# Kernel tuning notes

Hardware: AMD Instinct MI355X
Metric: run time of the kernel (lower is better)

Reference implementation:

```python
import jax, jax.numpy as jnp
import numpy as np

B, SQ, SKV = 4, 2048, 2048
DQ, DKV, H, NH = 1024, 1024, 1024, 16
HD = H // NH


def setup_inputs() -> dict:
    key = jax.random.key(0)
    ks = jax.random.split(key, 10)
    s = 0.02
    return {
        "query": jax.random.normal(ks[0], (B, SQ, DQ), jnp.float32),
        "key_value": jax.random.normal(ks[1], (B, SKV, DKV), jnp.float32),
        "Wq": jax.random.normal(ks[2], (DQ, H), jnp.float32) * s,
        "bq": jnp.zeros((H,), jnp.float32),
        "Wk": jax.random.normal(ks[3], (DKV, H), jnp.float32) * s,
        "bk": jnp.zeros((H,), jnp.float32),
        "Wv": jax.random.normal(ks[4], (DKV, H), jnp.float32) * s,
        "bv": jnp.zeros((H,), jnp.float32),
        "Wo": jax.random.normal(ks[5], (H, DQ), jnp.float32) * s,
        "bo": jnp.zeros((DQ,), jnp.float32),
    }


def reference(query, key_value, Wq, bq, Wk, bk, Wv, bv, Wo, bo):
    b, sq, _ = query.shape
    skv = key_value.shape[1]
    scale = np.sqrt(HD).astype(np.float32)
    # project and split heads: [B, S, H] -> [B, NH, S, HD]
    q = (query @ Wq + bq).reshape(b, sq, NH, HD).transpose(0, 2, 1, 3)
    k = (key_value @ Wk + bk).reshape(b, skv, NH, HD).transpose(0, 2, 1, 3)
    v = (key_value @ Wv + bv).reshape(b, skv, NH, HD).transpose(0, 2, 1, 3)
    scores = jnp.einsum("bhqd,bhkd->bhqk", q, k) / scale
    attn = jax.nn.softmax(scores, axis=-1)
    out = jnp.einsum("bhqk,bhkd->bhqd", attn, v)
    out = out.transpose(0, 2, 1, 3).reshape(b, sq, NH * HD)
    return out @ Wo + bo
```

## Files before the change

kernel.cpp:

```cpp
#include <hip/hip_runtime.h>


typedef short s16x8 __attribute__((ext_vector_type(8)));
typedef short s16x4 __attribute__((ext_vector_type(4)));
typedef float f32x4 __attribute__((ext_vector_type(4)));
typedef float f32x16 __attribute__((ext_vector_type(16)));
typedef unsigned short u16;
typedef unsigned int u32;

__device__ __forceinline__ u16 f2bf(float f){
    union{float f;u32 u;} v; v.f=f;
    u32 r = v.u + 0x7fffu + ((v.u>>16)&1u);
    return (u16)(r>>16);
}
__device__ __forceinline__ int swz(int row,int colB){ return row*128 + (colB ^ ((row&7)<<4)); }

__device__ __forceinline__ void gl16(const void* g, void* l){
    __builtin_amdgcn_global_load_lds((__attribute__((address_space(1))) void*)(void*)g,
                                     (__attribute__((address_space(3))) void*)l, 16, 0, 0);
}
__device__ __forceinline__ u32 cvtpk(float lo, float hi){
    u32 r; asm("v_cvt_pk_bf16_f32 %0, %1, %2" : "=v"(r) : "v"(lo), "v"(hi)); return r;
}
__device__ __forceinline__ void plswap(u32& a, u32& b){
    asm("v_permlane32_swap_b32 %0, %1" : "+v"(a), "+v"(b));
}

#define QSCALE 0.1803368801111204f

__global__ __launch_bounds__(256) void cvtbf2(const float* __restrict__ a, const float* __restrict__ b,
                                              u16* __restrict__ oa, u16* __restrict__ ob){
    int blk = blockIdx.x;
    const float* in = a; u16* out = oa;
    if (blk >= 4096){ in = b; out = ob; blk -= 4096; }
    size_t i = ((size_t)blk*256 + threadIdx.x)*8;
    f32x4 x = *(const f32x4*)(in+i), y = *(const f32x4*)(in+i+4);
    s16x8 o;
    #pragma unroll
    for (int j=0;j<4;++j){ o[j]=(short)f2bf(x[j]); o[4+j]=(short)f2bf(y[j]); }
    *(s16x8*)(out+i) = o;
}

__device__ __forceinline__ void transW_body(const float* __restrict__ W, u16* __restrict__ Wt){
    __shared__ u16 T[64*68];
    const int tid = threadIdx.x;
    const int n0 = blockIdx.x*64, k0 = blockIdx.y*64;
    const int tr = tid>>4, tc = (tid&15)*4;
    #pragma unroll
    for (int p=0;p<4;++p){
        int k = p*16 + tr;
        f32x4 v = *(const f32x4*)(W + (size_t)(k0+k)*1024 + n0 + tc);
        s16x4 o;
        #pragma unroll
        for (int j=0;j<4;++j) o[j]=(short)f2bf(v[j]);
        *(s16x4*)(T + k*68 + tc) = o;
    }
    __syncthreads();
    #pragma unroll
    for (int p=0;p<4;++p){
        int n = p*16 + tr;
        s16x4 o;
        #pragma unroll
        for (int e=0;e<4;++e) o[e] = (short)T[(tc+e)*68 + n];
        *(s16x4*)(Wt + (size_t)(n0+n)*1024 + k0 + tc) = o;
    }
}
__global__ __launch_bounds__(256) void transW(const float* __restrict__ W, u16* __restrict__ Wt){
    transW_body(W, Wt);
}
__global__ __launch_bounds__(256) void transW3(const float* __restrict__ W0, const float* __restrict__ W1,
                                               const float* __restrict__ W2,
                                               u16* __restrict__ O0, u16* __restrict__ O1, u16* __restrict__ O2){
    const float* W = blockIdx.z==0 ? W0 : (blockIdx.z==1 ? W1 : W2);
    u16*       Wt = blockIdx.z==0 ? O0 : (blockIdx.z==1 ? O1 : O2);
    transW_body(W, Wt);
}

template<int EPI>
__global__ __launch_bounds__(256)
void gemm128(const u16* __restrict__ A, const u16* __restrict__ Bt,
             const float* __restrict__ bias, void* __restrict__ C,
             int M, int N, int K, float scale)
{
    __shared__ __align__(16) u16 As[2][128*64];
    __shared__ __align__(16) u16 Bs[2][128*64];
    const int tid = threadIdx.x, lane = tid&63, wave = tid>>6;
    const int ln = lane&15, g = lane>>4;
    const int wm = wave>>1, wn = wave&1;
    const int bm = blockIdx.x, bn = blockIdx.y;

    f32x4 acc[4][4] = {};

    const int r0g = tid>>3, cc8 = (tid&7)*8;
    const u16* aA = A  + (size_t)(bm*128 + r0g)*K + cc8;
    const u16* aB = Bt + (size_t)(bn*128 + r0g)*K + cc8;

    auto stage = [&](int k0, int buf){
        char* pa = (char*)As[buf] + tid*16;
        char* pb = (char*)Bs[buf] + tid*16;
        #pragma unroll
        for (int i=0;i<4;++i){
            gl16(aA + k0 + i*32*K, pa + i*4096);
            gl16(aB + k0 + i*32*K, pb + i*4096);
        }
    };

    stage(0, 0);
    int cur = 0;
    for (int k0=0; k0<K; k0+=64){
        if (k0+64 < K){
            stage(k0+64, cur^1);
            asm volatile("s_waitcnt vmcnt(8)" ::: "memory");
        } else {
            asm volatile("s_waitcnt vmcnt(0)" ::: "memory");
        }
        __builtin_amdgcn_s_barrier();
        #pragma unroll
        for (int kk=0;kk<2;++kk){
            s16x8 af[4], bf[4];
            #pragma unroll
            for (int mi=0;mi<4;++mi)
                af[mi] = *(const s16x8*)((const char*)As[cur] + (size_t)(wm*64+mi*16+ln)*128 + kk*64 + g*16);
            #pragma unroll
            for (int ni=0;ni<4;++ni)
                bf[ni] = *(const s16x8*)((const char*)Bs[cur] + (size_t)(wn*64+ni*16+ln)*128 + kk*64 + g*16);
            #pragma unroll
            for (int mi=0;mi<4;++mi)
                #pragma unroll
                for (int ni=0;ni<4;++ni)
                    acc[mi][ni] = __builtin_amdgcn_mfma_f32_16x16x32_bf16(af[mi], bf[ni], acc[mi][ni], 0,0,0);
        }
        __builtin_amdgcn_s_barrier();
        cur ^= 1;
    }

    #pragma unroll
    for (int mi=0;mi<4;++mi){
        #pragma unroll
        for (int ni=0;ni<4;++ni){
            int col = bn*128 + wn*64 + ni*16 + ln;
            float bv = bias[col];
            #pragma unroll
            for (int r=0;r<4;++r){
                int row = bm*128 + wm*64 + mi*16 + 4*g + r;
                float v = (acc[mi][ni][r] + bv) * scale;
                if constexpr (EPI==0)
                    ((u16*)C)[(size_t)row*N + col] = f2bf(v);
                else if constexpr (EPI==2){
                    int b = row>>11, s = row&2047;
                    ((u16*)C)[((size_t)(b*1024 + col))*2048 + s] = f2bf(v);
                } else
                    ((float*)C)[(size_t)row*N + col] = v;
            }
        }
    }
}

template<bool A_IS_F32, int EPI>
__global__ __launch_bounds__(256)
void gemm_bias_64(const void* __restrict__ Av, const float* __restrict__ W,
                  const float* __restrict__ bias, void* __restrict__ Cout,
                  int M, int N, int K, float scale)
{
    __shared__ __align__(16) char smem[16384];
    char* As = smem;
    char* Ws = smem + 8192;
    const int tid  = threadIdx.x;
    const int lane = tid & 63, wave = tid >> 6;
    const int g = lane >> 4, ln = lane & 15;
    const int wm = wave >> 1, wn = wave & 1;
    const int bm = blockIdx.x, bn = blockIdx.y;
    f32x4 acc[2][2] = {};
    const int srow = tid >> 2;
    const int sch  = (tid & 3) * 16;

    for (int k0 = 0; k0 < K; k0 += 64) {
        if constexpr (A_IS_F32) {
            const float* a = (const float*)Av + (size_t)(bm*64+srow)*K + k0 + sch;
            const f32x4* a4 = (const f32x4*)a;
            #pragma unroll
            for (int c = 0; c < 2; ++c) {
                f32x4 x = a4[c*2+0], y = a4[c*2+1];
                s16x8 wv;
                #pragma unroll
                for (int j = 0; j < 4; ++j){ wv[j]=(short)f2bf(x[j]); wv[4+j]=(short)f2bf(y[j]); }
                *(s16x8*)(As + swz(srow, sch*2 + c*16)) = wv;
            }
        } else {
            const u16* a = (const u16*)Av + (size_t)(bm*64+srow)*K + k0 + sch;
            *(s16x8*)(As + swz(srow, sch*2 + 0))  = *(const s16x8*)(a + 0);
            *(s16x8*)(As + swz(srow, sch*2 + 16)) = *(const s16x8*)(a + 8);
        }
        {
            const float* wsrc = W + (size_t)(k0+srow)*N + bn*64 + sch;
            #pragma unroll
            for (int j = 0; j < 16; ++j) {
                int n = sch + j;
                *(short*)(Ws + n*128 + ((srow*2) ^ ((n&7)<<4))) = (short)f2bf(wsrc[j]);
            }
        }
        __syncthreads();
        #pragma unroll
        for (int kk = 0; kk < 2; ++kk) {
            s16x8 af[2], bfr[2];
            #pragma unroll
            for (int mi = 0; mi < 2; ++mi)
                af[mi] = *(const s16x8*)(As + swz(wm*32+mi*16+ln, kk*64 + g*16));
            #pragma unroll
            for (int ni = 0; ni < 2; ++ni)
                bfr[ni] = *(const s16x8*)(Ws + swz(wn*32+ni*16+ln, kk*64 + g*16));
            #pragma unroll
            for (int mi = 0; mi < 2; ++mi)
                #pragma unroll
                for (int ni = 0; ni < 2; ++ni)
                    acc[mi][ni] = __builtin_amdgcn_mfma_f32_16x16x32_bf16(af[mi], bfr[ni], acc[mi][ni], 0,0,0);
        }
        __syncthreads();
    }
    #pragma unroll
    for (int mi = 0; mi < 2; ++mi){
        #pragma unroll
        for (int ni = 0; ni < 2; ++ni){
            int col = bn*64 + wn*32 + ni*16 + ln;
            float bv = bias[col];
            #pragma unroll
            for (int r = 0; r < 4; ++r){
                int row = bm*64 + wm*32 + mi*16 + 4*g + r;
                float v = (acc[mi][ni][r] + bv) * scale;
                if constexpr (EPI==0)
                    ((u16*)Cout)[(size_t)row*N + col] = f2bf(v);
                else if constexpr (EPI==2){
                    int b = row>>11, s = row&2047;
                    ((u16*)Cout)[((size_t)(b*1024+col))*2048 + s] = f2bf(v);
                } else
                    ((float*)Cout)[(size_t)row*N + col] = v;
            }
        }
    }
}

__global__ __launch_bounds__(256)
void attn_fwd5(const u16* __restrict__ Q, const u16* __restrict__ K,
               const u16* __restrict__ Vt, u16* __restrict__ O)
{
    __shared__ __align__(16) char smem[32768];
    const int tid = threadIdx.x, lane = tid&63, wave = tid>>6;
    const int l31 = lane&31, hl = lane>>5;

    int dlin = blockIdx.y*16 + blockIdx.x;
    int xc = dlin&7, t0 = dlin>>3;
    int bh = xc*8 + (t0>>4), qt = t0&15;
    int b = bh>>4, h = bh&15;

    const int qrow = qt*128 + wave*32 + l31;
    const size_t qgoff = ((size_t)(b*2048 + qrow))*1024 + h*64;
    const u16* Kg = K  + ((size_t)(b*2048))*1024 + h*64;
    const u16* Vg = Vt + ((size_t)(b*1024 + h*64))*2048;

    s16x8 bq[4];
    #pragma unroll
    for (int ks=0;ks<4;++ks)
        bq[ks] = *(const s16x8*)(Q + qgoff + 16*ks + 8*hl);

    float m_run = -1e30f, l_run = 0.0f;
    f32x16 oa0 = {}, oa1 = {};

    const int r0 = tid>>3;
    const int qc = (tid&7) ^ (r0&7);
    const u16* kbase = Kg + (size_t)r0*1024 + qc*8;
    const u16* vbase = Vg + (size_t)r0*2048 + qc*8;
    const int ldst = tid*16;

    auto stage = [&](int kt, int buf){
        char* Kb = smem + buf*16384;
        char* Vb = Kb + 8192;
        const size_t kkOff = (size_t)kt*65536;
        const int kv0 = kt*64;
        gl16(kbase + kkOff,           Kb + ldst);
        gl16(kbase + kkOff + 32768,   Kb + 4096 + ldst);
        gl16(vbase + kv0,             Vb + ldst);
        gl16(vbase + kv0 + 65536,     Vb + 4096 + ldst);
    };

    int kofs[8];
    #pragma unroll
    for (int hk=0;hk<2;++hk)
        #pragma unroll
        for (int ks=0;ks<4;++ks)
            kofs[hk*4+ks] = swz(hk*32 + l31, 32*ks + 16*hl);

    auto qk = [&](int buf, f32x16& sA, f32x16& sB){
        char* Kb = smem + buf*16384;
        f32x16 a = {}, c = {};
        __builtin_amdgcn_s_setprio(1);
        #pragma unroll
        for (int ks=0; ks<4; ++ks){
            s16x8 ak0 = *(const s16x8*)(Kb + kofs[ks]);
            s16x8 ak1 = *(const s16x8*)(Kb + kofs[4+ks]);
            a = __builtin_amdgcn_mfma_f32_32x32x16_bf16(ak0, bq[ks], a, 0,0,0);
            c = __builtin_amdgcn_mfma_f32_32x32x16_bf16(ak1, bq[ks], c, 0,0,0);
        }
        __builtin_amdgcn_s_setprio(0);
        sA = a; sB = c;
    };

    auto smpack = [&](f32x16& s0, f32x16& s1, s16x8* bP){
        float tm[8];
        #pragma unroll
        for (int i=0;i<8;++i) tm[i] = fmaxf(fmaxf(fmaxf(s0[i], s0[i+8]), s1[i]), s1[i+8]);
        float pm = fmaxf(fmaxf(fmaxf(tm[0],tm[1]),fmaxf(tm[2],tm[3])),
                         fmaxf(fmaxf(tm[4],tm[5]),fmaxf(tm[6],tm[7])));
        pm = fmaxf(pm, __shfl_xor(pm, 32));
        if (!__all(pm - m_run <= 8.0f)){
            float mn  = fmaxf(m_run, pm);
            float scl = __builtin_amdgcn_exp2f(m_run - mn);
            oa0 *= scl; oa1 *= scl;
            l_run *= scl;
            m_run = mn;
        }
        #pragma unroll
        for (int r=0; r<16; ++r){
            s0[r] = __builtin_amdgcn_exp2f(s0[r] - m_run);
            s1[r] = __builtin_amdgcn_exp2f(s1[r] - m_run);
        }
        float ts[8];
        #pragma unroll
        for (int i=0;i<8;++i) ts[i] = (s0[i]+s0[i+8]) + (s1[i]+s1[i+8]);
        float rs = ((ts[0]+ts[1])+(ts[2]+ts[3])) + ((ts[4]+ts[5])+(ts[6]+ts[7]));
        rs += __shfl_xor(rs, 32);
        l_run += rs;
        #pragma unroll
        for (int f=0; f<2; ++f){
            const f32x16& sf = f ? s1 : s0;
            u32 W[8];
            #pragma unroll
            for (int w=0; w<8; ++w) W[w] = cvtpk(sf[2*w], sf[2*w+1]);
            #pragma unroll
            for (int s=0; s<2; ++s){
                u32 x0 = W[4*s+0], y0 = W[4*s+2];
                u32 x1 = W[4*s+1], y1 = W[4*s+3];
                plswap(x0, y0);
                plswap(x1, y1);
                union { u32 w[4]; s16x8 v; } u;
                u.w[0]=x0; u.w[1]=x1; u.w[2]=y0; u.w[3]=y1;
                bP[2*f+s] = u.v;
            }
        }
    };

    auto pv = [&](int buf, const s16x8* bP){
        char* Vb = smem + buf*16384 + 8192;
        __builtin_amdgcn_s_setprio(1);
        #pragma unroll
        for (int ks=0; ks<4; ++ks){
            s16x8 av0 = *(const s16x8*)(Vb + kofs[ks]);
            s16x8 av1 = *(const s16x8*)(Vb + kofs[4+ks]);
            oa0 = __builtin_amdgcn_mfma_f32_32x32x16_bf16(av0, bP[ks], oa0, 0,0,0);
            oa1 = __builtin_amdgcn_mfma_f32_32x32x16_bf16(av1, bP[ks], oa1, 0,0,0);
        }
        __builtin_amdgcn_s_setprio(0);
    };

    int cur = 0;
    auto body = [&](f32x16& sC0, f32x16& sC1, f32x16& sN0, f32x16& sN1, int kt){
        asm volatile("s_waitcnt vmcnt(2)" ::: "memory");
        __builtin_amdgcn_s_barrier();
        qk(cur^1, sN0, sN1);
        s16x8 bP[4];
        smpack(sC0, sC1, bP);
        pv(cur, bP);
        __builtin_amdgcn_s_barrier();
        if (kt < 30) stage(kt+2, cur);
        cur ^= 1;
    };

    stage(0, 0);
    stage(1, 1);
    asm volatile("s_waitcnt vmcnt(6)" ::: "memory");
    __builtin_amdgcn_s_barrier();
    f32x16 sa, sb, sc, sd;
    qk(0, sa, sb);

    int kt = 0;
    #pragma unroll 1
    for (int it=0; it<15; ++it){
        body(sa, sb, sc, sd, kt); ++kt;
        body(sc, sd, sa, sb, kt); ++kt;
    }
    body(sa, sb, sc, sd, kt); ++kt;

    asm volatile("s_waitcnt vmcnt(0)" ::: "memory");
    __builtin_amdgcn_s_barrier();
    {
        s16x8 bP[4];
        smpack(sc, sd, bP);
        pv(cur, bP);
    }

    float inv = 1.0f / l_run;
    u16* Ob = O + qgoff;
    #pragma unroll
    for (int fd=0; fd<2; ++fd){
        const f32x16& oaf = fd ? oa1 : oa0;
        #pragma unroll
        for (int rq=0; rq<4; ++rq){
            s16x4 o;
            #pragma unroll
            for (int e=0;e<4;++e) o[e] = (short)f2bf(oaf[rq*4+e] * inv);
            *(s16x4*)(Ob + fd*32 + rq*8 + hl*4) = o;
        }
    }
}

extern "C" void kernel_launch(void* const* d_in, const int* in_sizes, int n_in,
                              void* d_out, int out_size, void* d_ws, size_t ws_size,
                              hipStream_t stream)
{
    const float* query = (const float*)d_in[0];
    const float* kvin  = (const float*)d_in[1];
    const float* Wq = (const float*)d_in[2];
    const float* bq = (const float*)d_in[3];
    const float* Wk = (const float*)d_in[4];
    const float* bk = (const float*)d_in[5];
    const float* Wv = (const float*)d_in[6];
    const float* bv = (const float*)d_in[7];
    const float* Wo = (const float*)d_in[8];
    const float* bo = (const float*)d_in[9];

    const int M = 8192, D = 1024;
    const size_t MB = 1024ull*1024ull;
    u16* Qb  = (u16*)d_ws;
    u16* Kb  = Qb  + 8*MB;
    u16* Vtb = Kb  + 8*MB;
    u16* Ob  = Vtb + 8*MB;

    if (ws_size >= 66*MB) {
        u16* Wt0  = Ob + 8*MB;
        u16* Wt1  = Ob;
        u16* Wt2  = Ob + 1*MB;
        u16* qbf  = (u16*)d_out;
        u16* kvbf = qbf + 8*MB;

        cvtbf2<<<8192,256,0,stream>>>(query, kvin, qbf, kvbf);

        dim3 tg3(16,16,3), tg(16,16), gg(64,8);
        transW3<<<tg3,256,0,stream>>>(Wq, Wk, Wv, Wt0, Wt1, Wt2);
        gemm128<0><<<gg,256,0,stream>>>(qbf,  Wt0, bq, Qb,  M, D, D, QSCALE);
        transW<<<tg,256,0,stream>>>(Wo, Wt0);
        gemm128<0><<<gg,256,0,stream>>>(kvbf, Wt1, bk, Kb,  M, D, D, 1.0f);
        gemm128<2><<<gg,256,0,stream>>>(kvbf, Wt2, bv, Vtb, M, D, D, 1.0f);

        attn_fwd5<<<dim3(16,64),256,0,stream>>>(Qb, Kb, Vtb, Ob);

        gemm128<3><<<gg,256,0,stream>>>(Ob, Wt0, bo, d_out, M, D, D, 1.0f);
    } else {
        dim3 gg(128,16);
        gemm_bias_64<true ,0><<<gg,256,0,stream>>>(query, Wq, bq, Qb,  M, D, D, QSCALE);
        gemm_bias_64<true ,0><<<gg,256,0,stream>>>(kvin,  Wk, bk, Kb,  M, D, D, 1.0f);
        gemm_bias_64<true ,2><<<gg,256,0,stream>>>(kvin,  Wv, bv, Vtb, M, D, D, 1.0f);
        attn_fwd5<<<dim3(16,64),256,0,stream>>>(Qb, Kb, Vtb, Ob);
        gemm_bias_64<false,3><<<gg,256,0,stream>>>(Ob, Wo, bo, d_out, M, D, D, 1.0f);
    }
}
```

Measured before the change: 230.3 us.

## Rewrite attention to load K/V directly into registers with 64 query rows per wave

```diff
diff --git a/kernel.cpp b/kernel.cpp
--- a/kernel.cpp
+++ b/kernel.cpp
@@ -25,6 +25,8 @@
 __device__ __forceinline__ void plswap(u32& a, u32& b){
     asm("v_permlane32_swap_b32 %0, %1" : "+v"(a), "+v"(b));
 }
+__device__ __forceinline__ float xmaxf(float v){ return fmaxf(v, __shfl_xor(v, 32)); }
+__device__ __forceinline__ float xsumf(float v){ return v + __shfl_xor(v, 32); }
 
 #define QSCALE 0.1803368801111204f
 
@@ -239,175 +241,149 @@
     }
 }
 
-__global__ __launch_bounds__(256)
-void attn_fwd5(const u16* __restrict__ Q, const u16* __restrict__ K,
+__global__ __launch_bounds__(256, 2)
+void attn_fwd7(const u16* __restrict__ Q, const u16* __restrict__ K,
                const u16* __restrict__ Vt, u16* __restrict__ O)
 {
-    __shared__ __align__(16) char smem[32768];
     const int tid = threadIdx.x, lane = tid&63, wave = tid>>6;
     const int l31 = lane&31, hl = lane>>5;
 
-    int dlin = blockIdx.y*16 + blockIdx.x;
-    int xc = dlin&7, t0 = dlin>>3;
-    int bh = xc*8 + (t0>>4), qt = t0&15;
+    int L = blockIdx.x;
+    int task = (L&7)*64 + (L>>3);
+    int bh = task>>3, qt = task&7;
     int b = bh>>4, h = bh&15;
 
-    const int qrow = qt*128 + wave*32 + l31;
-    const size_t qgoff = ((size_t)(b*2048 + qrow))*1024 + h*64;
+    const int q0 = qt*256 + wave*64;
     const u16* Kg = K  + ((size_t)(b*2048))*1024 + h*64;
     const u16* Vg = Vt + ((size_t)(b*1024 + h*64))*2048;
 
-    s16x8 bq[4];
-    #pragma unroll
-    for (int ks=0;ks<4;++ks)
-        bq[ks] = *(const s16x8*)(Q + qgoff + 16*ks + 8*hl);
-
-    float m_run = -1e30f, l_run = 0.0f;
-    f32x16 oa0 = {}, oa1 = {};
-
-    const int r0 = tid>>3;
-    const int qc = (tid&7) ^ (r0&7);
-    const u16* kbase = Kg + (size_t)r0*1024 + qc*8;
-    const u16* vbase = Vg + (size_t)r0*2048 + qc*8;
-    const int ldst = tid*16;
-
-    auto stage = [&](int kt, int buf){
-        char* Kb = smem + buf*16384;
-        char* Vb = Kb + 8192;
-        const size_t kkOff = (size_t)kt*65536;
-        const int kv0 = kt*64;
-        gl16(kbase + kkOff,           Kb + ldst);
-        gl16(kbase + kkOff + 32768,   Kb + 4096 + ldst);
-        gl16(vbase + kv0,             Vb + ldst);
-        gl16(vbase + kv0 + 65536,     Vb + 4096 + ldst);
-    };
-
-    int kofs[8];
-    #pragma unroll
-    for (int hk=0;hk<2;++hk)
-        #pragma unroll
-        for (int ks=0;ks<4;++ks)
-            kofs[hk*4+ks] = swz(hk*32 + l31, 32*ks + 16*hl);
-
-    auto qk = [&](int buf, f32x16& sA, f32x16& sB){
-        char* Kb = smem + buf*16384;
-        f32x16 a = {}, c = {};
+    size_t qoff0 = ((size_t)(b*2048 + q0      + l31))*1024 + h*64;
+    size_t qoff1 = ((size_t)(b*2048 + q0 + 32 + l31))*1024 + h*64;
+    s16x8 bq0[4], bq1[4];
+    #pragma unroll
+    for (int ks=0;ks<4;++ks){
+        bq0[ks] = *(const s16x8*)(Q + qoff0 + 16*ks + 8*hl);
+        bq1[ks] = *(const s16x8*)(Q + qoff1 + 16*ks + 8*hl);
+    }
+
+    float m0=-1e30f, m1=-1e30f, l0=0.0f, l1=0.0f;
+    f32x16 oa00={}, oa01={}, oa10={}, oa11={};
+
+    const u16* kp  = Kg + (size_t)l31*1024 + 8*hl;
+    const u16* vp0 = Vg + (size_t)l31*2048 + 8*hl;
+    const u16* vp1 = Vg + (size_t)(32+l31)*2048 + 8*hl;
+
+    auto loadK = [&](s16x8 (&kf)[4], int t){
+        const u16* p = kp + (size_t)t*32768;
+        #pragma unroll
+        for (int ks=0;ks<4;++ks) kf[ks] = *(const s16x8*)(p + 16*ks);
+    };
+    auto loadV = [&](s16x8 (&vf)[4], int t){
+        const u16* p0 = vp0 + t*32;
+        const u16* p1 = vp1 + t*32;
+        #pragma unroll
+        for (int ks=0;ks<2;++ks){
+            vf[ks]   = *(const s16x8*)(p0 + 16*ks);
+            vf[2+ks] = *(const s16x8*)(p1 + 16*ks);
+        }
+    };
+
+    auto rmax = [](const f32x16& s)->float{
+        float a = fmaxf(fmaxf(s[0],s[1]),fmaxf(s[2],s[3]));
+        float b2= fmaxf(fmaxf(s[4],s[5]),fmaxf(s[6],s[7]));
+        float c = fmaxf(fmaxf(s[8],s[9]),fmaxf(s[10],s[11]));
+        float d = fmaxf(fmaxf(s[12],s[13]),fmaxf(s[14],s[15]));
+        return fmaxf(fmaxf(a,b2),fmaxf(c,d));
+    };
+    auto rsum = [](const f32x16& s)->float{
+        float a=(s[0]+s[1])+(s[2]+s[3]), b2=(s[4]+s[5])+(s[6]+s[7]);
+        float c=(s[8]+s[9])+(s[10]+s[11]), d=(s[12]+s[13])+(s[14]+s[15]);
+        return (a+b2)+(c+d);
+    };
+    auto pack = [&](const f32x16& sf, s16x8 (&bP)[2]){
+        u32 W[8];
+        #pragma unroll
+        for (int w=0;w<8;++w) W[w] = cvtpk(sf[2*w], sf[2*w+1]);
+        #pragma unroll
+        for (int s=0;s<2;++s){
+            u32 x0=W[4*s+0], y0=W[4*s+2], x1=W[4*s+1], y1=W[4*s+3];
+            plswap(x0,y0); plswap(x1,y1);
+            union{u32 w[4]; s16x8 v;} u;
+            u.w[0]=x0; u.w[1]=x1; u.w[2]=y0; u.w[3]=y1;
+            bP[s]=u.v;
+        }
+    };
+
+    auto compute = [&](const s16x8 (&kf)[4], const s16x8 (&vf)[4]){
+        f32x16 s0={}, s1={};
         __builtin_amdgcn_s_setprio(1);
         #pragma unroll
-        for (int ks=0; ks<4; ++ks){
-            s16x8 ak0 = *(const s16x8*)(Kb + kofs[ks]);
-            s16x8 ak1 = *(const s16x8*)(Kb + kofs[4+ks]);
-            a = __builtin_amdgcn_mfma_f32_32x32x16_bf16(ak0, bq[ks], a, 0,0,0);
-            c = __builtin_amdgcn_mfma_f32_32x32x16_bf16(ak1, bq[ks], c, 0,0,0);
+        for (int ks=0;ks<4;++ks){
+            s0 = __builtin_amdgcn_mfma_f32_32x32x16_bf16(kf[ks], bq0[ks], s0, 0,0,0);
+            s1 = __builtin_amdgcn_mfma_f32_32x32x16_bf16(kf[ks], bq1[ks], s1, 0,0,0);
         }
         __builtin_amdgcn_s_setprio(0);
-        sA = a; sB = c;
-    };
-
-    auto smpack = [&](f32x16& s0, f32x16& s1, s16x8* bP){
-        float tm[8];
-        #pragma unroll
-        for (int i=0;i<8;++i) tm[i] = fmaxf(fmaxf(fmaxf(s0[i], s0[i+8]), s1[i]), s1[i+8]);
-        float pm = fmaxf(fmaxf(fmaxf(tm[0],tm[1]),fmaxf(tm[2],tm[3])),
-                         fmaxf(fmaxf(tm[4],tm[5]),fmaxf(tm[6],tm[7])));
-        pm = fmaxf(pm, __shfl_xor(pm, 32));
-        if (!__all(pm - m_run <= 8.0f)){
-            float mn  = fmaxf(m_run, pm);
-            float scl = __builtin_amdgcn_exp2f(m_run - mn);
-            oa0 *= scl; oa1 *= scl;
-            l_run *= scl;
-            m_run = mn;
-        }
-        #pragma unroll
-        for (int r=0; r<16; ++r){
-            s0[r] = __builtin_amdgcn_exp2f(s0[r] - m_run);
-            s1[r] = __builtin_amdgcn_exp2f(s1[r] - m_run);
-        }
-        float ts[8];
-        #pragma unroll
-        for (int i=0;i<8;++i) ts[i] = (s0[i]+s0[i+8]) + (s1[i]+s1[i+8]);
-        float rs = ((ts[0]+ts[1])+(ts[2]+ts[3])) + ((ts[4]+ts[5])+(ts[6]+ts[7]));
-        rs += __shfl_xor(rs, 32);
-        l_run += rs;
-        #pragma unroll
-        for (int f=0; f<2; ++f){
-            const f32x16& sf = f ? s1 : s0;
-            u32 W[8];
-            #pragma unroll
-            for (int w=0; w<8; ++w) W[w] = cvtpk(sf[2*w], sf[2*w+1]);
-            #pragma unroll
-            for (int s=0; s<2; ++s){
-                u32 x0 = W[4*s+0], y0 = W[4*s+2];
-                u32 x1 = W[4*s+1], y1 = W[4*s+3];
-                plswap(x0, y0);
-                plswap(x1, y1);
-                union { u32 w[4]; s16x8 v; } u;
-                u.w[0]=x0; u.w[1]=x1; u.w[2]=y0; u.w[3]=y1;
-                bP[2*f+s] = u.v;
+
+        float pm0 = xmaxf(rmax(s0));
+        float pm1 = xmaxf(rmax(s1));
+        if (!__all(pm0 - m0 <= 8.0f && pm1 - m1 <= 8.0f)){
+            float mn0 = fmaxf(m0, pm0), mn1 = fmaxf(m1, pm1);
+            float c0 = __builtin_amdgcn_exp2f(m0 - mn0);
+            float c1 = __builtin_amdgcn_exp2f(m1 - mn1);
+            oa00 *= c0; oa01 *= c0; oa10 *= c1; oa11 *= c1;
+            l0 *= c0; l1 *= c1; m0 = mn0; m1 = mn1;
+        }
+        #pragma unroll
+        for (int r=0;r<16;++r){
+            s0[r] = __builtin_amdgcn_exp2f(s0[r] - m0);
+            s1[r] = __builtin_amdgcn_exp2f(s1[r] - m1);
+        }
+        l0 += xsumf(rsum(s0));
+        l1 += xsumf(rsum(s1));
+
+        s16x8 bP0[2], bP1[2];
+        pack(s0, bP0);
+        pack(s1, bP1);
+
+        __builtin_amdgcn_s_setprio(1);
+        #pragma unroll
+        for (int ks=0;ks<2;++ks){
+            oa00 = __builtin_amdgcn_mfma_f32_32x32x16_bf16(vf[ks],   bP0[ks], oa00, 0,0,0);
+            oa01 = __builtin_amdgcn_mfma_f32_32x32x16_bf16(vf[2+ks], bP0[ks], oa01, 0,0,0);
+            oa10 = __builtin_amdgcn_mfma_f32_32x32x16_bf16(vf[ks],   bP1[ks], oa10, 0,0,0);
+            oa11 = __builtin_amdgcn_mfma_f32_32x32x16_bf16(vf[2+ks], bP1[ks], oa11, 0,0,0);
+        }
+        __builtin_amdgcn_s_setprio(0);
+    };
+
+    s16x8 kfA[4], vfA[4], kfB[4], vfB[4];
+    loadK(kfA, 0); loadV(vfA, 0);
+    #pragma unroll 1
+    for (int it=0; it<32; ++it){
+        int t = 2*it;
+        loadK(kfB, t+1); loadV(vfB, t+1);
+        compute(kfA, vfA);
+        if (it < 31){ loadK(kfA, t+2); loadV(vfA, t+2); }
+        compute(kfB, vfB);
+    }
+
+    float inv0 = 1.0f / l0, inv1 = 1.0f / l1;
+    u16* Ob0 = O + qoff0;
+    u16* Ob1 = O + qoff1;
+    #pragma unroll
+    for (int fd=0; fd<2; ++fd){
+        const f32x16& a0 = fd ? oa01 : oa00;
+        const f32x16& a1 = fd ? oa11 : oa10;
+        #pragma unroll
+        for (int rq=0; rq<4; ++rq){
+            s16x4 o0, o1;
+            #pragma unroll
+            for (int e=0;e<4;++e){
+                o0[e] = (short)f2bf(a0[rq*4+e] * inv0);
+                o1[e] = (short)f2bf(a1[rq*4+e] * inv1);
             }
-        }
-    };
-
-    auto pv = [&](int buf, const s16x8* bP){
-        char* Vb = smem + buf*16384 + 8192;
-        __builtin_amdgcn_s_setprio(1);
-        #pragma unroll
-        for (int ks=0; ks<4; ++ks){
-            s16x8 av0 = *(const s16x8*)(Vb + kofs[ks]);
-            s16x8 av1 = *(const s16x8*)(Vb + kofs[4+ks]);
-            oa0 = __builtin_amdgcn_mfma_f32_32x32x16_bf16(av0, bP[ks], oa0, 0,0,0);
-            oa1 = __builtin_amdgcn_mfma_f32_32x32x16_bf16(av1, bP[ks], oa1, 0,0,0);
-        }
-        __builtin_amdgcn_s_setprio(0);
-    };
-
-    int cur = 0;
-    auto body = [&](f32x16& sC0, f32x16& sC1, f32x16& sN0, f32x16& sN1, int kt){
-        asm volatile("s_waitcnt vmcnt(2)" ::: "memory");
-        __builtin_amdgcn_s_barrier();
-        qk(cur^1, sN0, sN1);
-        s16x8 bP[4];
-        smpack(sC0, sC1, bP);
-        pv(cur, bP);
-        __builtin_amdgcn_s_barrier();
-        if (kt < 30) stage(kt+2, cur);
-        cur ^= 1;
-    };
-
-    stage(0, 0);
-    stage(1, 1);
-    asm volatile("s_waitcnt vmcnt(6)" ::: "memory");
-    __builtin_amdgcn_s_barrier();
-    f32x16 sa, sb, sc, sd;
-    qk(0, sa, sb);
-
-    int kt = 0;
-    #pragma unroll 1
-    for (int it=0; it<15; ++it){
-        body(sa, sb, sc, sd, kt); ++kt;
-        body(sc, sd, sa, sb, kt); ++kt;
-    }
-    body(sa, sb, sc, sd, kt); ++kt;
-
-    asm volatile("s_waitcnt vmcnt(0)" ::: "memory");
-    __builtin_amdgcn_s_barrier();
-    {
-        s16x8 bP[4];
-        smpack(sc, sd, bP);
-        pv(cur, bP);
-    }
-
-    float inv = 1.0f / l_run;
-    u16* Ob = O + qgoff;
-    #pragma unroll
-    for (int fd=0; fd<2; ++fd){
-        const f32x16& oaf = fd ? oa1 : oa0;
-        #pragma unroll
-        for (int rq=0; rq<4; ++rq){
-            s16x4 o;
-            #pragma unroll
-            for (int e=0;e<4;++e) o[e] = (short)f2bf(oaf[rq*4+e] * inv);
-            *(s16x4*)(Ob + fd*32 + rq*8 + hl*4) = o;
+            *(s16x4*)(Ob0 + fd*32 + rq*8 + hl*4) = o0;
+            *(s16x4*)(Ob1 + fd*32 + rq*8 + hl*4) = o1;
         }
     }
 }
@@ -450,7 +426,7 @@
         gemm128<0><<<gg,256,0,stream>>>(kvbf, Wt1, bk, Kb,  M, D, D, 1.0f);
         gemm128<2><<<gg,256,0,stream>>>(kvbf, Wt2, bv, Vtb, M, D, D, 1.0f);
 
-        attn_fwd5<<<dim3(16,64),256,0,stream>>>(Qb, Kb, Vtb, Ob);
+        attn_fwd7<<<512,256,0,stream>>>(Qb, Kb, Vtb, Ob);
 
         gemm128<3><<<gg,256,0,stream>>>(Ob, Wt0, bo, d_out, M, D, D, 1.0f);
     } else {
@@ -458,7 +434,7 @@
         gemm_bias_64<true ,0><<<gg,256,0,stream>>>(query, Wq, bq, Qb,  M, D, D, QSCALE);
         gemm_bias_64<true ,0><<<gg,256,0,stream>>>(kvin,  Wk, bk, Kb,  M, D, D, 1.0f);
         gemm_bias_64<true ,2><<<gg,256,0,stream>>>(kvin,  Wv, bv, Vtb, M, D, D, 1.0f);
-        attn_fwd5<<<dim3(16,64),256,0,stream>>>(Qb, Kb, Vtb, Ob);
+        attn_fwd7<<<512,256,0,stream>>>(Qb, Kb, Vtb, Ob);
         gemm_bias_64<false,3><<<gg,256,0,stream>>>(Ob, Wo, bo, d_out, M, D, D, 1.0f);
     }
 }
```

Result: slower. 255.7 us (+11.1%).

## Fuse input conversion and weight transposes into one prep kernel; stage V-transpose epilogue via LDS

Applied to the files above, without the earlier changes.

```diff
diff --git a/kernel.cpp b/kernel.cpp
--- a/kernel.cpp
+++ b/kernel.cpp
@@ -28,23 +28,10 @@
 
 #define QSCALE 0.1803368801111204f
 
-__global__ __launch_bounds__(256) void cvtbf2(const float* __restrict__ a, const float* __restrict__ b,
-                                              u16* __restrict__ oa, u16* __restrict__ ob){
-    int blk = blockIdx.x;
-    const float* in = a; u16* out = oa;
-    if (blk >= 4096){ in = b; out = ob; blk -= 4096; }
-    size_t i = ((size_t)blk*256 + threadIdx.x)*8;
-    f32x4 x = *(const f32x4*)(in+i), y = *(const f32x4*)(in+i+4);
-    s16x8 o;
-    #pragma unroll
-    for (int j=0;j<4;++j){ o[j]=(short)f2bf(x[j]); o[4+j]=(short)f2bf(y[j]); }
-    *(s16x8*)(out+i) = o;
-}
-
-__device__ __forceinline__ void transW_body(const float* __restrict__ W, u16* __restrict__ Wt){
+__device__ __forceinline__ void transW_body(const float* __restrict__ W, u16* __restrict__ Wt,
+                                            int n0, int k0){
     __shared__ u16 T[64*68];
     const int tid = threadIdx.x;
-    const int n0 = blockIdx.x*64, k0 = blockIdx.y*64;
     const int tr = tid>>4, tc = (tid&15)*4;
     #pragma unroll
     for (int p=0;p<4;++p){
@@ -65,15 +52,32 @@
         *(s16x4*)(Wt + (size_t)(n0+n)*1024 + k0 + tc) = o;
     }
 }
-__global__ __launch_bounds__(256) void transW(const float* __restrict__ W, u16* __restrict__ Wt){
-    transW_body(W, Wt);
-}
-__global__ __launch_bounds__(256) void transW3(const float* __restrict__ W0, const float* __restrict__ W1,
-                                               const float* __restrict__ W2,
-                                               u16* __restrict__ O0, u16* __restrict__ O1, u16* __restrict__ O2){
-    const float* W = blockIdx.z==0 ? W0 : (blockIdx.z==1 ? W1 : W2);
-    u16*       Wt = blockIdx.z==0 ? O0 : (blockIdx.z==1 ? O1 : O2);
-    transW_body(W, Wt);
+
+__global__ __launch_bounds__(256)
+void prep(const float* __restrict__ q, const float* __restrict__ kv,
+          u16* __restrict__ qbf, u16* __restrict__ kvbf,
+          const float* __restrict__ W0, const float* __restrict__ W1,
+          const float* __restrict__ W2, const float* __restrict__ W3,
+          u16* __restrict__ T0, u16* __restrict__ T1,
+          u16* __restrict__ T2, u16* __restrict__ T3)
+{
+    int blk = blockIdx.x;
+    if (blk < 8192){
+        const float* in = q; u16* out = qbf;
+        if (blk >= 4096){ in = kv; out = kvbf; blk -= 4096; }
+        size_t i = ((size_t)blk*256 + threadIdx.x)*8;
+        f32x4 x = *(const f32x4*)(in+i), y = *(const f32x4*)(in+i+4);
+        s16x8 o;
+        #pragma unroll
+        for (int j=0;j<4;++j){ o[j]=(short)f2bf(x[j]); o[4+j]=(short)f2bf(y[j]); }
+        *(s16x8*)(out+i) = o;
+    } else {
+        blk -= 8192;
+        int w = blk>>8, rem = blk&255;
+        const float* W = (w==0)?W0:(w==1)?W1:(w==2)?W2:W3;
+        u16*      Wt  = (w==0)?T0:(w==1)?T1:(w==2)?T2:T3;
+        transW_body(W, Wt, (rem&15)*64, (rem>>4)*64);
+    }
 }
 
 template<int EPI>
@@ -134,24 +138,220 @@
         cur ^= 1;
     }
 
-    #pragma unroll
-    for (int mi=0;mi<4;++mi){
-        #pragma unroll
-        for (int ni=0;ni<4;++ni){
-            int col = bn*128 + wn*64 + ni*16 + ln;
-            float bv = bias[col];
-            #pragma unroll
-            for (int r=0;r<4;++r){
-                int row = bm*128 + wm*64 + mi*16 + 4*g + r;
-                float v = (acc[mi][ni][r] + bv) * scale;
-                if constexpr (EPI==0)
-                    ((u16*)C)[(size_t)row*N + col] = f2bf(v);
-                else if constexpr (EPI==2){
-                    int b = row>>11, s = row&2047;
-                    ((u16*)C)[((size_t)(b*1024 + col))*2048 + s] = f2bf(v);
-                } else
-                    ((float*)C)[(size_t)row*N + col] = v;
-            }
+    if constexpr (EPI==2){
+        u16* T = (u16*)As;
+        #pragma unroll
+        for (int mi=0;mi<4;++mi){
+            #pragma unroll
+            for (int ni=0;ni<4;++ni){
+                int colp = wn*64 + ni*16 + ln;
+                int row0 = wm*64 + mi*16 + 4*g;
+                float bv = bias[bn*128 + colp];
+                s16x4 pk4;
+                #pragma unroll
+                for (int r=0;r<4;++r) pk4[r] = (short)f2bf(acc[mi][ni][r] + bv);
+                *(s16x4*)((char*)T + colp*256 + ((row0*2) ^ ((colp&7)<<4))) = pk4;
+            }
+        }
+        __syncthreads();
+        const int cold = tid>>1, chunk = (tid&1)*64;
+        const int b = bm>>4, sbase = (bm*128)&2047;
+        u16* dst = (u16*)C + ((size_t)(b*1024 + bn*128 + cold))*2048 + sbase + chunk;
+        #pragma unroll
+        for (int i=0;i<8;++i){
+            s16x8 vv = *(const s16x8*)((char*)T + cold*256 + (((chunk + i*8)*2) ^ ((cold&7)<<4)));
+            *(s16x8*)(dst + i*8) = vv;
+        }
+    } else {
+        #pragma unroll
+        for (int mi=0;mi<4;++mi){
+            #pragma unroll
+            for (int ni=0;ni<4;++ni){
+                int col = bn*128 + wn*64 + ni*16 + ln;
+                float bv = bias[col];
+                #pragma unroll
+                for (int r=0;r<4;++r){
+                    int row = bm*128 + wm*64 + mi*16 + 4*g + r;
+                    float v = (acc[mi][ni][r] + bv) * scale;
+                    if constexpr (EPI==0)
+                        ((u16*)C)[(size_t)row*N + col] = f2bf(v);
+                    else
+                        ((float*)C)[(size_t)row*N + col] = v;
+                }
+            }
+        }
+    }
+}
+
+__global__ __launch_bounds__(256)
+void attn_fwd9(const u16* __restrict__ Q, const u16* __restrict__ K,
+               const u16* __restrict__ Vt, u16* __restrict__ O)
+{
+    __shared__ __align__(16) char smem[32768];
+    const int tid = threadIdx.x, lane = tid&63, wave = tid>>6;
+    const int l31 = lane&31, hl = lane>>5;
+
+    int dlin = blockIdx.y*16 + blockIdx.x;
+    int xc = dlin&7, t0 = dlin>>3;
+    int bh = xc*8 + (t0>>4), qt = t0&15;
+    int b = bh>>4, h = bh&15;
+
+    const int qrow = qt*128 + wave*32 + l31;
+    const size_t qgoff = ((size_t)(b*2048 + qrow))*1024 + h*64;
+    const u16* Kg = K  + ((size_t)(b*2048))*1024 + h*64;
+    const u16* Vg = Vt + ((size_t)(b*1024 + h*64))*2048;
+
+    s16x8 bq[4];
+    #pragma unroll
+    for (int ks=0;ks<4;++ks)
+        bq[ks] = *(const s16x8*)(Q + qgoff + 16*ks + 8*hl);
+
+    float m_run = -1e30f, l_run = 0.0f;
+    f32x16 oa0 = {}, oa1 = {};
+
+    const int r0 = tid>>3;
+    const int qc = (tid&7) ^ (r0&7);
+    const u16* kbase = Kg + (size_t)r0*1024 + qc*8;
+    const u16* vbase = Vg + (size_t)r0*2048 + qc*8;
+    const int ldst = tid*16;
+
+    auto stage = [&](int kt, int buf){
+        char* Kb = smem + buf*16384;
+        char* Vb = Kb + 8192;
+        const size_t kkOff = (size_t)kt*65536;
+        const int kv0 = kt*64;
+        gl16(kbase + kkOff,           Kb + ldst);
+        gl16(kbase + kkOff + 32768,   Kb + 4096 + ldst);
+        gl16(vbase + kv0,             Vb + ldst);
+        gl16(vbase + kv0 + 65536,     Vb + 4096 + ldst);
+    };
+
+    int kofs[8];
+    #pragma unroll
+    for (int hk=0;hk<2;++hk)
+        #pragma unroll
+        for (int ks=0;ks<4;++ks)
+            kofs[hk*4+ks] = swz(hk*32 + l31, 32*ks + 16*hl);
+
+    auto qk = [&](int buf, f32x16& sA, f32x16& sB){
+        char* Kb = smem + buf*16384;
+        f32x16 a = {}, c = {};
+        __builtin_amdgcn_s_setprio(1);
+        #pragma unroll
+        for (int ks=0; ks<4; ++ks){
+            s16x8 ak0 = *(const s16x8*)(Kb + kofs[ks]);
+            s16x8 ak1 = *(const s16x8*)(Kb + kofs[4+ks]);
+            a = __builtin_amdgcn_mfma_f32_32x32x16_bf16(ak0, bq[ks], a, 0,0,0);
+            c = __builtin_amdgcn_mfma_f32_32x32x16_bf16(ak1, bq[ks], c, 0,0,0);
+        }
+        __builtin_amdgcn_s_setprio(0);
+        sA = a; sB = c;
+    };
+
+    auto smpack = [&](f32x16& s0, f32x16& s1, s16x8* bP){
+        float tm[8];
+        #pragma unroll
+        for (int i=0;i<8;++i) tm[i] = fmaxf(fmaxf(fmaxf(s0[i], s0[i+8]), s1[i]), s1[i+8]);
+        float pm = fmaxf(fmaxf(fmaxf(tm[0],tm[1]),fmaxf(tm[2],tm[3])),
+                         fmaxf(fmaxf(tm[4],tm[5]),fmaxf(tm[6],tm[7])));
+        pm = fmaxf(pm, __shfl_xor(pm, 32));
+        if (!__all(pm - m_run <= 8.0f)){
+            float mn  = fmaxf(m_run, pm);
+            float scl = __builtin_amdgcn_exp2f(m_run - mn);
+            oa0 *= scl; oa1 *= scl;
+            l_run *= scl;
+            m_run = mn;
+        }
+        #pragma unroll
+        for (int r=0; r<16; ++r){
+            s0[r] = __builtin_amdgcn_exp2f(s0[r] - m_run);
+            s1[r] = __builtin_amdgcn_exp2f(s1[r] - m_run);
+        }
+        float ts[8];
+        #pragma unroll
+        for (int i=0;i<8;++i) ts[i] = (s0[i]+s0[i+8]) + (s1[i]+s1[i+8]);
+        float rs = ((ts[0]+ts[1])+(ts[2]+ts[3])) + ((ts[4]+ts[5])+(ts[6]+ts[7]));
+        rs += __shfl_xor(rs, 32);
+        l_run += rs;
+        #pragma unroll
+        for (int f=0; f<2; ++f){
+            const f32x16& sf = f ? s1 : s0;
+            u32 W[8];
+            #pragma unroll
+            for (int w=0; w<8; ++w) W[w] = cvtpk(sf[2*w], sf[2*w+1]);
+            #pragma unroll
+            for (int s=0; s<2; ++s){
+                u32 x0 = W[4*s+0], y0 = W[4*s+2];
+                u32 x1 = W[4*s+1], y1 = W[4*s+3];
+                plswap(x0, y0);
+                plswap(x1, y1);
+                union { u32 w[4]; s16x8 v; } u;
+                u.w[0]=x0; u.w[1]=x1; u.w[2]=y0; u.w[3]=y1;
+                bP[2*f+s] = u.v;
+            }
+        }
+    };
+
+    auto pv = [&](int buf, const s16x8* bP){
+        char* Vb = smem + buf*16384 + 8192;
+        __builtin_amdgcn_s_setprio(1);
+        #pragma unroll
+        for (int ks=0; ks<4; ++ks){
+            s16x8 av0 = *(const s16x8*)(Vb + kofs[ks]);
+            s16x8 av1 = *(const s16x8*)(Vb + kofs[4+ks]);
+            oa0 = __builtin_amdgcn_mfma_f32_32x32x16_bf16(av0, bP[ks], oa0, 0,0,0);
+            oa1 = __builtin_amdgcn_mfma_f32_32x32x16_bf16(av1, bP[ks], oa1, 0,0,0);
+        }
+        __builtin_amdgcn_s_setprio(0);
+    };
+
+    int cur = 0;
+    auto body = [&](f32x16& sC0, f32x16& sC1, f32x16& sN0, f32x16& sN1, int kt){
+        asm volatile("s_waitcnt vmcnt(2)" ::: "memory");
+        __builtin_amdgcn_s_barrier();
+        qk(cur^1, sN0, sN1);
+        s16x8 bP[4];
+        smpack(sC0, sC1, bP);
+        pv(cur, bP);
+        __builtin_amdgcn_s_barrier();
+        if (kt < 30) stage(kt+2, cur);
+        cur ^= 1;
+    };
+
+    stage(0, 0);
+    stage(1, 1);
+    asm volatile("s_waitcnt vmcnt(6)" ::: "memory");
+    __builtin_amdgcn_s_barrier();
+    f32x16 sa, sb, sc, sd;
+    qk(0, sa, sb);
+
+    int kt = 0;
+    #pragma unroll 1
+    for (int it=0; it<15; ++it){
+        body(sa, sb, sc, sd, kt); ++kt;
+        body(sc, sd, sa, sb, kt); ++kt;
+    }
+    body(sa, sb, sc, sd, kt); ++kt;
+
+    asm volatile("s_waitcnt vmcnt(0)" ::: "memory");
+    __builtin_amdgcn_s_barrier();
+    {
+        s16x8 bP[4];
+        smpack(sc, sd, bP);
+        pv(cur, bP);
+    }
+
+    float inv = 1.0f / l_run;
+    u16* Ob = O + qgoff;
+    #pragma unroll
+    for (int fd=0; fd<2; ++fd){
+        const f32x16& oaf = fd ? oa1 : oa0;
+        #pragma unroll
+        for (int rq=0; rq<4; ++rq){
+            s16x4 o;
+            #pragma unroll
+            for (int e=0;e<4;++e) o[e] = (short)f2bf(oaf[rq*4+e] * inv);
+            *(s16x4*)(Ob + fd*32 + rq*8 + hl*4) = o;
         }
     }
 }
@@ -239,179 +439,6 @@
     }
 }
 
-__global__ __launch_bounds__(256)
-void attn_fwd5(const u16* __restrict__ Q, const u16* __restrict__ K,
-               const u16* __restrict__ Vt, u16* __restrict__ O)
-{
-    __shared__ __align__(16) char smem[32768];
-    const int tid = threadIdx.x, lane = tid&63, wave = tid>>6;
-    const int l31 = lane&31, hl = lane>>5;
-
-    int dlin = blockIdx.y*16 + blockIdx.x;
-    int xc = dlin&7, t0 = dlin>>3;
-    int bh = xc*8 + (t0>>4), qt = t0&15;
-    int b = bh>>4, h = bh&15;
-
-    const int qrow = qt*128 + wave*32 + l31;
-    const size_t qgoff = ((size_t)(b*2048 + qrow))*1024 + h*64;
-    const u16* Kg = K  + ((size_t)(b*2048))*1024 + h*64;
-    const u16* Vg = Vt + ((size_t)(b*1024 + h*64))*2048;
-
-    s16x8 bq[4];
-    #pragma unroll
-    for (int ks=0;ks<4;++ks)
-        bq[ks] = *(const s16x8*)(Q + qgoff + 16*ks + 8*hl);
-
-    float m_run = -1e30f, l_run = 0.0f;
-    f32x16 oa0 = {}, oa1 = {};
-
-    const int r0 = tid>>3;
-    const int qc = (tid&7) ^ (r0&7);
-    const u16* kbase = Kg + (size_t)r0*1024 + qc*8;
-    const u16* vbase = Vg + (size_t)r0*2048 + qc*8;
-    const int ldst = tid*16;
-
-    auto stage = [&](int kt, int buf){
-        char* Kb = smem + buf*16384;
-        char* Vb = Kb + 8192;
-        const size_t kkOff = (size_t)kt*65536;
-        const int kv0 = kt*64;
-        gl16(kbase + kkOff,           Kb + ldst);
-        gl16(kbase + kkOff + 32768,   Kb + 4096 + ldst);
-        gl16(vbase + kv0,             Vb + ldst);
-        gl16(vbase + kv0 + 65536,     Vb + 4096 + ldst);
-    };
-
-    int kofs[8];
-    #pragma unroll
-    for (int hk=0;hk<2;++hk)
-        #pragma unroll
-        for (int ks=0;ks<4;++ks)
-            kofs[hk*4+ks] = swz(hk*32 + l31, 32*ks + 16*hl);
-
-    auto qk = [&](int buf, f32x16& sA, f32x16& sB){
-        char* Kb = smem + buf*16384;
-        f32x16 a = {}, c = {};
-        __builtin_amdgcn_s_setprio(1);
-        #pragma unroll
-        for (int ks=0; ks<4; ++ks){
-            s16x8 ak0 = *(const s16x8*)(Kb + kofs[ks]);
-            s16x8 ak1 = *(const s16x8*)(Kb + kofs[4+ks]);
-            a = __builtin_amdgcn_mfma_f32_32x32x16_bf16(ak0, bq[ks], a, 0,0,0);
-            c = __builtin_amdgcn_mfma_f32_32x32x16_bf16(ak1, bq[ks], c, 0,0,0);
-        }
-        __builtin_amdgcn_s_setprio(0);
-        sA = a; sB = c;
-    };
-
-    auto smpack = [&](f32x16& s0, f32x16& s1, s16x8* bP){
-        float tm[8];
-        #pragma unroll
-        for (int i=0;i<8;++i) tm[i] = fmaxf(fmaxf(fmaxf(s0[i], s0[i+8]), s1[i]), s1[i+8]);
-        float pm = fmaxf(fmaxf(fmaxf(tm[0],tm[1]),fmaxf(tm[2],tm[3])),
-                         fmaxf(fmaxf(tm[4],tm[5]),fmaxf(tm[6],tm[7])));
-        pm = fmaxf(pm, __shfl_xor(pm, 32));
-        if (!__all(pm - m_run <= 8.0f)){
-            float mn  = fmaxf(m_run, pm);
-            float scl = __builtin_amdgcn_exp2f(m_run - mn);
-            oa0 *= scl; oa1 *= scl;
-            l_run *= scl;
-            m_run = mn;
-        }
-        #pragma unroll
-        for (int r=0; r<16; ++r){
-            s0[r] = __builtin_amdgcn_exp2f(s0[r] - m_run);
-            s1[r] = __builtin_amdgcn_exp2f(s1[r] - m_run);
-        }
-        float ts[8];
-        #pragma unroll
-        for (int i=0;i<8;++i) ts[i] = (s0[i]+s0[i+8]) + (s1[i]+s1[i+8]);
-        float rs = ((ts[0]+ts[1])+(ts[2]+ts[3])) + ((ts[4]+ts[5])+(ts[6]+ts[7]));
-        rs += __shfl_xor(rs, 32);
-        l_run += rs;
-        #pragma unroll
-        for (int f=0; f<2; ++f){
-            const f32x16& sf = f ? s1 : s0;
-            u32 W[8];
-            #pragma unroll
-            for (int w=0; w<8; ++w) W[w] = cvtpk(sf[2*w], sf[2*w+1]);
-            #pragma unroll
-            for (int s=0; s<2; ++s){
-                u32 x0 = W[4*s+0], y0 = W[4*s+2];
-                u32 x1 = W[4*s+1], y1 = W[4*s+3];
-                plswap(x0, y0);
-                plswap(x1, y1);
-                union { u32 w[4]; s16x8 v; } u;
-                u.w[0]=x0; u.w[1]=x1; u.w[2]=y0; u.w[3]=y1;
-                bP[2*f+s] = u.v;
-            }
-        }
-    };
-
-    auto pv = [&](int buf, const s16x8* bP){
-        char* Vb = smem + buf*16384 + 8192;
-        __builtin_amdgcn_s_setprio(1);
-        #pragma unroll
-        for (int ks=0; ks<4; ++ks){
-            s16x8 av0 = *(const s16x8*)(Vb + kofs[ks]);
-            s16x8 av1 = *(const s16x8*)(Vb + kofs[4+ks]);
-            oa0 = __builtin_amdgcn_mfma_f32_32x32x16_bf16(av0, bP[ks], oa0, 0,0,0);
-            oa1 = __builtin_amdgcn_mfma_f32_32x32x16_bf16(av1, bP[ks], oa1, 0,0,0);
-        }
-        __builtin_amdgcn_s_setprio(0);
-    };
-
-    int cur = 0;
-    auto body = [&](f32x16& sC0, f32x16& sC1, f32x16& sN0, f32x16& sN1, int kt){
-        asm volatile("s_waitcnt vmcnt(2)" ::: "memory");
-        __builtin_amdgcn_s_barrier();
-        qk(cur^1, sN0, sN1);
-        s16x8 bP[4];
-        smpack(sC0, sC1, bP);
-        pv(cur, bP);
-        __builtin_amdgcn_s_barrier();
-        if (kt < 30) stage(kt+2, cur);
-        cur ^= 1;
-    };
-
-    stage(0, 0);
-    stage(1, 1);
-    asm volatile("s_waitcnt vmcnt(6)" ::: "memory");
-    __builtin_amdgcn_s_barrier();
-    f32x16 sa, sb, sc, sd;
-    qk(0, sa, sb);
-
-    int kt = 0;
-    #pragma unroll 1
-    for (int it=0; it<15; ++it){
-        body(sa, sb, sc, sd, kt); ++kt;
-        body(sc, sd, sa, sb, kt); ++kt;
-    }
-    body(sa, sb, sc, sd, kt); ++kt;
-
-    asm volatile("s_waitcnt vmcnt(0)" ::: "memory");
-    __builtin_amdgcn_s_barrier();
-    {
-        s16x8 bP[4];
-        smpack(sc, sd, bP);
-        pv(cur, bP);
-    }
-
-    float inv = 1.0f / l_run;
-    u16* Ob = O + qgoff;
-    #pragma unroll
-    for (int fd=0; fd<2; ++fd){
-        const f32x16& oaf = fd ? oa1 : oa0;
-        #pragma unroll
-        for (int rq=0; rq<4; ++rq){
-            s16x4 o;
-            #pragma unroll
-            for (int e=0;e<4;++e) o[e] = (short)f2bf(oaf[rq*4+e] * inv);
-            *(s16x4*)(Ob + fd*32 + rq*8 + hl*4) = o;
-        }
-    }
-}
-
 extern "C" void kernel_launch(void* const* d_in, const int* in_sizes, int n_in,
                               void* d_out, int out_size, void* d_ws, size_t ws_size,
                               hipStream_t stream)
@@ -435,30 +462,30 @@
     u16* Ob  = Vtb + 8*MB;
 
     if (ws_size >= 66*MB) {
-        u16* Wt0  = Ob + 8*MB;
-        u16* Wt1  = Ob;
-        u16* Wt2  = Ob + 1*MB;
+        u16* Wtq = Ob;
+        u16* Wtk = Ob + 1*MB;
+        u16* Wtv = Ob + 2*MB;
+        u16* Wto = Ob + 8*MB;
         u16* qbf  = (u16*)d_out;
         u16* kvbf = qbf + 8*MB;
 
-        cvtbf2<<<8192,256,0,stream>>>(query, kvin, qbf, kvbf);
-
-        dim3 tg3(16,16,3), tg(16,16), gg(64,8);
-        transW3<<<tg3,256,0,stream>>>(Wq, Wk, Wv, Wt0, Wt1, Wt2);
-        gemm128<0><<<gg,256,0,stream>>>(qbf,  Wt0, bq, Qb,  M, D, D, QSCALE);
-        transW<<<tg,256,0,stream>>>(Wo, Wt0);
-        gemm128<0><<<gg,256,0,stream>>>(kvbf, Wt1, bk, Kb,  M, D, D, 1.0f);
-        gemm128<2><<<gg,256,0,stream>>>(kvbf, Wt2, bv, Vtb, M, D, D, 1.0f);
-
-        attn_fwd5<<<dim3(16,64),256,0,stream>>>(Qb, Kb, Vtb, Ob);
-
-        gemm128<3><<<gg,256,0,stream>>>(Ob, Wt0, bo, d_out, M, D, D, 1.0f);
+        prep<<<9216,256,0,stream>>>(query, kvin, qbf, kvbf,
+                                    Wq, Wk, Wv, Wo, Wtq, Wtk, Wtv, Wto);
+
+        dim3 gg(64,8);
+        gemm128<0><<<gg,256,0,stream>>>(qbf,  Wtq, bq, Qb,  M, D, D, QSCALE);
+        gemm128<0><<<gg,256,0,stream>>>(kvbf, Wtk, bk, Kb,  M, D, D, 1.0f);
+        gemm128<2><<<gg,256,0,stream>>>(kvbf, Wtv, bv, Vtb, M, D, D, 1.0f);
+
+        attn_fwd9<<<dim3(16,64),256,0,stream>>>(Qb, Kb, Vtb, Ob);
+
+        gemm128<3><<<gg,256,0,stream>>>(Ob, Wto, bo, d_out, M, D, D, 1.0f);
     } else {
         dim3 gg(128,16);
         gemm_bias_64<true ,0><<<gg,256,0,stream>>>(query, Wq, bq, Qb,  M, D, D, QSCALE);
         gemm_bias_64<true ,0><<<gg,256,0,stream>>>(kvin,  Wk, bk, Kb,  M, D, D, 1.0f);
         gemm_bias_64<true ,2><<<gg,256,0,stream>>>(kvin,  Wv, bv, Vtb, M, D, D, 1.0f);
-        attn_fwd5<<<dim3(16,64),256,0,stream>>>(Qb, Kb, Vtb, Ob);
+        attn_fwd9<<<dim3(16,64),256,0,stream>>>(Qb, Kb, Vtb, Ob);
         gemm_bias_64<false,3><<<gg,256,0,stream>>>(Ob, Wo, bo, d_out, M, D, D, 1.0f);
     }
 }
```

New measurement: 226.5 us. About the same (-1.7%).
